# Kernel optimization log

Measured on AMD Instinct MI355X. Metric: run time of the kernel, lower is better.

The kernel has to match this reference:

```python
import jax, jax.numpy as jnp
import numpy as np


def _make_stencil():
    # Fixed finite-difference kernels from the torch module __init__
    w = np.zeros((4, 1, 3, 3), np.float32)
    w[0, 0, 1, 1] = 1.0; w[0, 0, 1, 2] = -1.0   # self - right
    w[1, 0, 1, 0] = 1.0; w[1, 0, 1, 1] = -1.0   # left - self
    w[2, 0, 1, 1] = 1.0; w[2, 0, 2, 1] = -1.0   # self - down
    w[3, 0, 0, 1] = 1.0; w[3, 0, 1, 1] = -1.0   # up - self
    return jnp.asarray(w)


def setup_inputs() -> dict:
    key = jax.random.key(0)
    H, W, S = 2160, 3840, 512
    seg = jax.random.randint(key, (1, 1, H, W), 0, S, dtype=jnp.int32)
    return {"seg": seg, "w": _make_stencil(), "num_segments": S}


def reference(seg, w, num_segments):
    S = int(num_segments)
    H, W_ = seg.shape[2], seg.shape[3]
    x = seg.astype(jnp.float32)
    # Conv2d(padding=3, padding_mode='replicate'): edge-pad by 3 then VALID 3x3 conv
    xp = jnp.pad(x, ((0, 0), (0, 0), (3, 3), (3, 3)), mode='edge')
    res = jax.lax.conv_general_dilated(
        xp, w, window_strides=(1, 1), padding='VALID',
        dimension_numbers=('NCHW', 'OIHW', 'NCHW'))  # (1,4,H+4,W+4)
    bm = (res != 0)[0, :, 2:-2, 2:-2]  # (4,H,W); boundary masks per direction

    s2 = seg[0, 0]  # (H,W) int
    # In the torch code, the k-th True of mask0 at (y,x) pairs with the k-th True
    # of mask1 at (y,x+1) (mask1 is mask0 shifted by +1 in x; replicate padding
    # guarantees equal counts). Hence horizontal edges are (seg[y,x], seg[y,x+1])
    # where bm[0], and vertical edges (seg[y,x], seg[y+1,x]) where bm[2].
    right_nb = jnp.concatenate([s2[:, 1:], s2[:, -1:]], axis=1)
    down_nb = jnp.concatenate([s2[1:, :], s2[-1:, :]], axis=0)

    flat = s2.ravel()
    adj = jnp.zeros((S, S), jnp.float32)
    adj = adj.at[flat, right_nb.ravel()].add(bm[0].astype(jnp.float32).ravel())
    adj = adj.at[flat, down_nb.ravel()].add(bm[2].astype(jnp.float32).ravel())
    # unique pairs -> presence matrix; diagonal (self-pairs) never occurs in original
    adj = jnp.where(adj > 0, 1.0, 0.0) * (1.0 - jnp.eye(S, dtype=jnp.float32))

    # centers(): per-segment mean of (x_index, y_index) -- the torch permute
    # reverses dims so column 0 is the W-axis mean, column 1 the H-axis mean.
    ys = jnp.broadcast_to(jnp.arange(H, dtype=jnp.float32)[:, None], (H, W_)).ravel()
    xs = jnp.broadcast_to(jnp.arange(W_, dtype=jnp.float32)[None, :], (H, W_)).ravel()
    cnt = jax.ops.segment_sum(jnp.ones_like(xs), flat, num_segments=S)
    sx = jax.ops.segment_sum(xs, flat, num_segments=S)
    sy = jax.ops.segment_sum(ys, flat, num_segments=S)
    centers = jnp.stack([sx, sy], axis=1) / cnt[:, None]
    return adj, centers
```

## Files before the change

kernel.cpp:

```cpp
#include <hip/hip_runtime.h>

#define HH 2160
#define WW 3840
#define SS 512
#define NW (SS * SS / 32)
#define NB 512

typedef unsigned int uint;
typedef unsigned long long ull;

__global__ __launch_bounds__(512) void seg_main(
    const int* __restrict__ seg, uint* __restrict__ wsOr,
    uint* __restrict__ part, int nb) {
  __shared__ uint s_bm[NW];
  __shared__ ull  s_pk[SS];
  for (int i = threadIdx.x; i < NW; i += 512) s_bm[i] = 0u;
  for (int i = threadIdx.x; i < SS; i += 512) s_pk[i] = 0ULL;
  __syncthreads();

  const int NC  = HH * WW / 4;
  const int cpb = (NC + nb - 1) / nb;
  const int c0  = blockIdx.x * cpb;
  const int c1  = min(c0 + cpb, NC);
  const int y0  = (c0 * 4) / WW;
  const int lane = threadIdx.x & 63;

  const int4* __restrict__ seg4  = (const int4*)seg;
  const int4* __restrict__ seg4d = (const int4*)(seg + WW);

  for (int c = c0 + threadIdx.x; c < c1; c += 512) {
    const int p = c * 4;
    const int y = p / WW;
    const int x = p - y * WW;
    const int4 v = seg4[c];
    const int4 d = (y < HH - 1) ? seg4d[c] : v;
    const int nshfl = __shfl_down(v.x, 1, 64);
    const bool need_load = (lane == 63) || (c + 1 >= c1);
    const int  a4 = min(p + 4, HH * WW - 1);
    const int  nxt = (x >= WW - 4) ? v.w : (need_load ? seg[a4] : nshfl);

    if (v.x != v.y) { int i = v.x * SS + v.y; atomicOr(&s_bm[i >> 5], 1u << (i & 31)); }
    if (v.y != v.z) { int i = v.y * SS + v.z; atomicOr(&s_bm[i >> 5], 1u << (i & 31)); }
    if (v.z != v.w) { int i = v.z * SS + v.w; atomicOr(&s_bm[i >> 5], 1u << (i & 31)); }
    if (v.w != nxt) { int i = v.w * SS + nxt; atomicOr(&s_bm[i >> 5], 1u << (i & 31)); }
    if (v.x != d.x) { int i = v.x * SS + d.x; atomicOr(&s_bm[i >> 5], 1u << (i & 31)); }
    if (v.y != d.y) { int i = v.y * SS + d.y; atomicOr(&s_bm[i >> 5], 1u << (i & 31)); }
    if (v.z != d.z) { int i = v.z * SS + d.z; atomicOr(&s_bm[i >> 5], 1u << (i & 31)); }
    if (v.w != d.w) { int i = v.w * SS + d.w; atomicOr(&s_bm[i >> 5], 1u << (i & 31)); }

    const ull yp = (1ULL << 48) | ((ull)(uint)x << 20) | (ull)(uint)(y - y0);
    atomicAdd(&s_pk[v.x], yp);
    atomicAdd(&s_pk[v.y], yp + (1ULL << 20));
    atomicAdd(&s_pk[v.z], yp + (2ULL << 20));
    atomicAdd(&s_pk[v.w], yp + (3ULL << 20));
  }
  __syncthreads();

  for (int i = threadIdx.x; i < NW; i += 512) {
    const uint m = s_bm[i];
    if (m) atomicOr(&wsOr[i], m);
  }
  for (int i = threadIdx.x; i < SS; i += 512) {
    const ull pk = s_pk[i];
    const uint cnt = (uint)(pk >> 48);
    const uint sx  = (uint)((pk >> 20) & 0x0FFFFFFFu);
    const uint sy  = (uint)(pk & 0xFFFFFu) + cnt * (uint)y0;
    part[(0 * SS + i) * nb + blockIdx.x] = cnt;
    part[(1 * SS + i) * nb + blockIdx.x] = sx;
    part[(2 * SS + i) * nb + blockIdx.x] = sy;
  }
}

__global__ __launch_bounds__(256) void finalize(
    const uint* __restrict__ wsOr, const uint* __restrict__ part, int nb,
    float* __restrict__ adj, float* __restrict__ centers) {
  const int g = blockIdx.x;
  const int t = threadIdx.x;

  if (g < 256) {
    const int q4 = g * 256 + t;
    const uint nib = (wsOr[q4 >> 3] >> ((q4 & 7) * 4)) & 0xFu;
    float4 o;
    o.x = (nib & 1u) ? 1.0f : 0.0f;
    o.y = (nib & 2u) ? 1.0f : 0.0f;
    o.z = (nib & 4u) ? 1.0f : 0.0f;
    o.w = (nib & 8u) ? 1.0f : 0.0f;
    ((float4*)adj)[q4] = o;
  } else {
    const int s = (g - 256) * 64 + (t >> 2);
    const int q = t & 3;
    ull cnt = 0, sx = 0, sy = 0;
    for (int b = q; b < nb; b += 4) {
      cnt += part[(0 * SS + s) * nb + b];
      sx  += part[(1 * SS + s) * nb + b];
      sy  += part[(2 * SS + s) * nb + b];
    }
    cnt += __shfl_down(cnt, 2, 4); cnt += __shfl_down(cnt, 1, 4);
    sx  += __shfl_down(sx,  2, 4); sx  += __shfl_down(sx,  1, 4);
    sy  += __shfl_down(sy,  2, 4); sy  += __shfl_down(sy,  1, 4);
    if (q == 0) {
      const double dc = (double)cnt;
      centers[s * 2 + 0] = (float)((double)sx / dc);
      centers[s * 2 + 1] = (float)((double)sy / dc);
    }
  }
}

extern "C" void kernel_launch(void* const* d_in, const int* in_sizes, int n_in,
                              void* d_out, int out_size, void* d_ws, size_t ws_size,
                              hipStream_t stream) {
  const int* seg = (const int*)d_in[0];
  float* out = (float*)d_out;
  float* adj = out;
  float* centers = out + SS * SS;

  uint* wsOr = (uint*)d_ws;
  uint* part = wsOr + NW;

  int nb = NB;
  const size_t need = (size_t)NW * 4 + (size_t)3 * SS * nb * 4;
  if (ws_size < need) {
    nb = (int)((ws_size - (size_t)NW * 4) / ((size_t)3 * SS * 4));
    if (nb > NB) nb = NB;
    if (nb < 256) nb = 256;
  }

  hipMemsetAsync(wsOr, 0, (size_t)NW * 4, stream);
  seg_main<<<nb, 512, 0, stream>>>(seg, wsOr, part, nb);
  finalize<<<256 + SS / 64, 256, 0, stream>>>(wsOr, part, nb, adj, centers);
}
```

Baseline: 132.3 us.

## Use grid-stride partitioning and split x-sum into separate shared atomic array

Replaces the contiguous per-block chunking with a grid-stride loop, drops the wavefront shuffle used to fetch the right neighbour in favour of a direct global load, and splits the packed 64-bit count/x/y accumulator into a 64-bit count+y word plus a separate 32-bit x-sum array. The repacking removes the per-block y offset trick so y sums fit without a base row. It doubles the number of shared atomics for centroid accumulation and loses the spatial locality of contiguous chunks, which likely raises shared-memory atomic contention and bitmap diversity per block.

```diff
diff --git a/kernel.cpp b/kernel.cpp
--- a/kernel.cpp
+++ b/kernel.cpp
@@ -14,30 +14,23 @@
     uint* __restrict__ part, int nb) {
   __shared__ uint s_bm[NW];
   __shared__ ull  s_pk[SS];
-  for (int i = threadIdx.x; i < NW; i += 512) s_bm[i] = 0u;
-  for (int i = threadIdx.x; i < SS; i += 512) s_pk[i] = 0ULL;
+  __shared__ uint s_sx[SS];
+  for (int i = threadIdx.x; i < NW; i += blockDim.x) s_bm[i] = 0u;
+  for (int i = threadIdx.x; i < SS; i += blockDim.x) { s_pk[i] = 0ULL; s_sx[i] = 0u; }
   __syncthreads();
 
-  const int NC  = HH * WW / 4;
-  const int cpb = (NC + nb - 1) / nb;
-  const int c0  = blockIdx.x * cpb;
-  const int c1  = min(c0 + cpb, NC);
-  const int y0  = (c0 * 4) / WW;
-  const int lane = threadIdx.x & 63;
-
+  const int NC = HH * WW / 4;
+  const int stride = gridDim.x * blockDim.x;
   const int4* __restrict__ seg4  = (const int4*)seg;
   const int4* __restrict__ seg4d = (const int4*)(seg + WW);
 
-  for (int c = c0 + threadIdx.x; c < c1; c += 512) {
+  for (int c = blockIdx.x * blockDim.x + threadIdx.x; c < NC; c += stride) {
     const int p = c * 4;
     const int y = p / WW;
     const int x = p - y * WW;
     const int4 v = seg4[c];
     const int4 d = (y < HH - 1) ? seg4d[c] : v;
-    const int nshfl = __shfl_down(v.x, 1, 64);
-    const bool need_load = (lane == 63) || (c + 1 >= c1);
-    const int  a4 = min(p + 4, HH * WW - 1);
-    const int  nxt = (x >= WW - 4) ? v.w : (need_load ? seg[a4] : nshfl);
+    const int nxt = (x < WW - 4) ? seg[p + 4] : v.w;
 
     if (v.x != v.y) { int i = v.x * SS + v.y; atomicOr(&s_bm[i >> 5], 1u << (i & 31)); }
     if (v.y != v.z) { int i = v.y * SS + v.z; atomicOr(&s_bm[i >> 5], 1u << (i & 31)); }
@@ -48,26 +41,23 @@
     if (v.z != d.z) { int i = v.z * SS + d.z; atomicOr(&s_bm[i >> 5], 1u << (i & 31)); }
     if (v.w != d.w) { int i = v.w * SS + d.w; atomicOr(&s_bm[i >> 5], 1u << (i & 31)); }
 
-    const ull yp = (1ULL << 48) | ((ull)(uint)x << 20) | (ull)(uint)(y - y0);
-    atomicAdd(&s_pk[v.x], yp);
-    atomicAdd(&s_pk[v.y], yp + (1ULL << 20));
-    atomicAdd(&s_pk[v.z], yp + (2ULL << 20));
-    atomicAdd(&s_pk[v.w], yp + (3ULL << 20));
+    const ull yp = (1ULL << 40) | (ull)(uint)y;
+    atomicAdd(&s_pk[v.x], yp); atomicAdd(&s_sx[v.x], (uint)x);
+    atomicAdd(&s_pk[v.y], yp); atomicAdd(&s_sx[v.y], (uint)(x + 1));
+    atomicAdd(&s_pk[v.z], yp); atomicAdd(&s_sx[v.z], (uint)(x + 2));
+    atomicAdd(&s_pk[v.w], yp); atomicAdd(&s_sx[v.w], (uint)(x + 3));
   }
   __syncthreads();
 
-  for (int i = threadIdx.x; i < NW; i += 512) {
-    const uint m = s_bm[i];
-    if (m) atomicOr(&wsOr[i], m);
+  for (int i = threadIdx.x; i < NW; i += blockDim.x) {
+    const uint val = s_bm[i];
+    if (val) atomicOr(&wsOr[i], val);
   }
-  for (int i = threadIdx.x; i < SS; i += 512) {
+  for (int i = threadIdx.x; i < SS; i += blockDim.x) {
     const ull pk = s_pk[i];
-    const uint cnt = (uint)(pk >> 48);
-    const uint sx  = (uint)((pk >> 20) & 0x0FFFFFFFu);
-    const uint sy  = (uint)(pk & 0xFFFFFu) + cnt * (uint)y0;
-    part[(0 * SS + i) * nb + blockIdx.x] = cnt;
-    part[(1 * SS + i) * nb + blockIdx.x] = sx;
-    part[(2 * SS + i) * nb + blockIdx.x] = sy;
+    part[(0 * SS + i) * nb + blockIdx.x] = (uint)(pk >> 40);
+    part[(1 * SS + i) * nb + blockIdx.x] = s_sx[i];
+    part[(2 * SS + i) * nb + blockIdx.x] = (uint)(pk & ((1ULL << 40) - 1));
   }
 }
 
@@ -122,7 +112,7 @@
   if (ws_size < need) {
     nb = (int)((ws_size - (size_t)NW * 4) / ((size_t)3 * SS * 4));
     if (nb > NB) nb = NB;
-    if (nb < 256) nb = 256;
+    if (nb < 1) nb = 1;
   }
 
   hipMemsetAsync(wsOr, 0, (size_t)NW * 4, stream);
```

After: 131.9 us. No clear change (-0.3%).
